# Kernel optimization log

Measured on AMD Instinct MI355X. Metric: run time of the kernel, lower is better.

Reference implementation:

```python
import jax, jax.numpy as jnp
import numpy as np

H = 16          # n_heads
MAX_REL = 512   # max_relative_positions


def setup_inputs() -> dict:
    key = jax.random.key(0)
    ks = jax.random.split(key, 8)
    B, S, D = 8, 512, 1024
    x = jax.random.normal(ks[0], (B, S, D), jnp.float32)
    rel_embeddings = jax.random.normal(ks[1], (2 * MAX_REL, D), jnp.float32) * 0.02
    Wq = jax.random.normal(ks[2], (D, D), jnp.float32) * 0.02
    Wk = jax.random.normal(ks[3], (D, D), jnp.float32) * 0.02
    Wv = jax.random.normal(ks[4], (D, D), jnp.float32) * 0.02
    bq = jnp.zeros((D,), jnp.float32)
    bk = jnp.zeros((D,), jnp.float32)
    bv = jnp.zeros((D,), jnp.float32)
    ids = jnp.arange(S)
    relative_pos = (ids[:, None] - ids[None, :]).astype(jnp.int32)  # q_id - k_id
    mask = jnp.ones((B, S), dtype=bool)
    return dict(x=x, rel_embeddings=rel_embeddings, Wq=Wq, bq=bq, Wk=Wk, bk=bk,
                Wv=Wv, bv=bv, relative_pos=relative_pos, mask=mask)


def _proj(t, W, b):
    # (..., D) -> (H, ..., W): linear + split heads + transpose_type '2013'
    y = t @ W.T + b
    y = y.reshape(*t.shape[:-1], H, y.shape[-1] // H)
    return jnp.moveaxis(y, -2, 0)


def reference(x, rel_embeddings, Wq, bq, Wk, bk, Wv, bv, relative_pos, mask):
    B, S, D = x.shape
    Wd = D // H
    span = S  # att_span = q_len
    scale = 1.0 / np.sqrt(Wd * 3.0)  # (head_size*(1+|pos_att_type|))**-0.5

    q = _proj(x, Wq, bq)  # (H,B,S,W)
    k = _proj(x, Wk, bk)
    v = _proj(x, Wv, bv)

    # relative position embeddings window [max_rel-span : max_rel+span]
    re = rel_embeddings[MAX_REL - span:MAX_REL + span]  # (2*span, D)
    pos_k = _proj(re, Wk, bk)  # (H, 2*span, W)
    pos_q = _proj(re, Wq, bq)  # (H, 2*span, W)

    # content-to-content scores
    scores = jnp.einsum('hbiw,hbjw->hbij', q, k) * scale  # (H,B,S,S)

    # c2p: query vs relative-position keys, gathered by rel index
    c2p = jnp.einsum('hbiw,hrw->hbir', q, pos_k) * scale  # (H,B,S,2*span)
    idx_c2p = jnp.clip(relative_pos + span - 1, 0, 2 * span - 1)  # (S,S)
    bias_c2p = jnp.take_along_axis(
        c2p, jnp.broadcast_to(idx_c2p[None, None], (H, B, S, S)), axis=-1)

    # p2c: key vs relative-position queries, gathered then transposed
    p2c = jnp.einsum('hbjw,hrw->hbjr', k, pos_q) * scale  # (H,B,S,2*span)
    idx_p2c = jnp.clip(-relative_pos + span - 1, 0, 2 * span - 1)
    g = jnp.take_along_axis(
        p2c, jnp.broadcast_to(idx_p2c[None, None], (H, B, S, S)), axis=-1)
    bias_p2c = jnp.swapaxes(g, -1, -2)  # (H,B,S(q),S(k))

    scores = scores + bias_c2p + bias_p2c
    scores = jnp.where(mask[None, :, None, :], scores, jnp.float32(-1e9))
    probs = jax.nn.softmax(scores, axis=-1)
    ctx = jnp.einsum('hbij,hbjw->hbiw', probs, v)  # (H,B,S,W)
    return jnp.transpose(ctx, (1, 2, 0, 3)).reshape(B, S, D)
```

## Files before the change

kernel.cpp:

```cpp
#include <hip/hip_runtime.h>


typedef __bf16 bf16_t;
typedef __bf16 bf16x8 __attribute__((ext_vector_type(8)));
typedef __bf16 bf16x4 __attribute__((ext_vector_type(4)));
typedef float  f32x4  __attribute__((ext_vector_type(4)));

#define MFMA16(a, b, c) __builtin_amdgcn_mfma_f32_16x16x32_bf16((a), (b), (c), 0, 0, 0)
#define S2SCALE 0.10411754f
#define MCONST  4.3280851f

__device__ __forceinline__ void gload_lds16(const bf16_t* g, bf16_t* lds) {
  __builtin_amdgcn_global_load_lds(
      (const __attribute__((address_space(1))) void*)g,
      (__attribute__((address_space(3))) void*)lds, 16, 0, 0);
}

__device__ __forceinline__ int kchunk(int row, int kg) {
  return row * 8 + (kg ^ (row & 7));
}

__global__ __launch_bounds__(256) void cvt_all(
    const float* __restrict__ x, const float* __restrict__ rel,
    const float* __restrict__ wq, const float* __restrict__ wk, const float* __restrict__ wv,
    bf16_t* __restrict__ out) {
  const size_t i = ((size_t)blockIdx.x * 256 + threadIdx.x) * 8;
  const float* src; size_t off;
  if (i < 4194304) { src = x; off = i; }
  else {
    size_t j = i - 4194304; int sel = (int)(j >> 20); off = j & 1048575;
    src = sel == 0 ? wq : sel == 1 ? wk : sel == 2 ? wv : rel;
  }
  float4 v0 = *reinterpret_cast<const float4*>(src + off);
  float4 v1 = *reinterpret_cast<const float4*>(src + off + 4);
  bf16x8 o;
  o[0] = (bf16_t)v0.x; o[1] = (bf16_t)v0.y; o[2] = (bf16_t)v0.z; o[3] = (bf16_t)v0.w;
  o[4] = (bf16_t)v1.x; o[5] = (bf16_t)v1.y; o[6] = (bf16_t)v1.z; o[7] = (bf16_t)v1.w;
  *reinterpret_cast<bf16x8*>(out + i) = o;
}

__device__ __forceinline__ void stage_tile(const bf16_t* base, int T, bf16_t* lds, int tid) {
#pragma unroll
  for (int i = 0; i < 2; ++i) {
    const int c = tid + i * 512;
    const int row = c >> 2, kg = (c & 3) ^ (row & 3);
    gload_lds16(base + (size_t)row * 1024 + T * 32 + kg * 8, lds + c * 8);
  }
}

#define VMW2 asm volatile("s_waitcnt vmcnt(2)" ::: "memory")
#define VMW0 asm volatile("s_waitcnt vmcnt(0)" ::: "memory")
#define NOPS ((void)0)

#define PH_BODY(AB, BB, FH, READB, STAGE_STMT, WAIT_STMT)                               \
  {                                                                                     \
    if (READB) {                                                                        \
      _Pragma("unroll") for (int n_ = 0; n_ < 4; ++n_)                                  \
        bfr[n_] = *reinterpret_cast<const bf16x8*>(                                     \
            (BB) + (((wn * 64 + n_ * 16 + li) * 4 + (gr ^ (li & 3))) * 8));             \
    }                                                                                   \
    bf16x8 af_[4];                                                                      \
    _Pragma("unroll") for (int a_ = 0; a_ < 4; ++a_)                                    \
      af_[a_] = *reinterpret_cast<const bf16x8*>(                                       \
          (AB) + (((wm * 128 + ((FH) * 4 + a_) * 16 + li) * 4 + (gr ^ (li & 3))) * 8)); \
    STAGE_STMT;                                                                         \
    __builtin_amdgcn_s_barrier();                                                       \
    asm volatile("s_waitcnt lgkmcnt(0)" ::: "memory");                                  \
    __builtin_amdgcn_sched_barrier(0);                                                  \
    __builtin_amdgcn_s_setprio(1);                                                      \
    _Pragma("unroll") for (int a_ = 0; a_ < 4; ++a_)                                    \
      _Pragma("unroll") for (int n_ = 0; n_ < 4; ++n_)                                  \
        acc[(FH) * 4 + a_][n_] = MFMA16(af_[a_], bfr[n_], acc[(FH) * 4 + a_][n_]);      \
    __builtin_amdgcn_s_setprio(0);                                                      \
    WAIT_STMT;                                                                          \
    __builtin_amdgcn_s_barrier();                                                       \
    __builtin_amdgcn_sched_barrier(0);                                                  \
  }

__global__ __launch_bounds__(512, 2) void gemm_qkv(
    const bf16_t* __restrict__ xb, const bf16_t* __restrict__ reb,
    const bf16_t* __restrict__ wqb, const bf16_t* __restrict__ wkb, const bf16_t* __restrict__ wvb,
    const float* __restrict__ bq, const float* __restrict__ bk, const float* __restrict__ bv,
    bf16_t* __restrict__ qo, bf16_t* __restrict__ ko, bf16_t* __restrict__ vo,
    bf16_t* __restrict__ pko, bf16_t* __restrict__ pqo) {
  __shared__ bf16_t Abuf[2][8192];
  __shared__ bf16_t Bbuf[2][8192];

  const int bid0 = blockIdx.x;
  const int bid = (bid0 & 7) * 28 + (bid0 >> 3);
  const int tid = threadIdx.x;
  const int wave = tid >> 6;
  const int wm = wave >> 2, wn = wave & 3;
  const int l = tid & 63, li = l & 15, gr = l >> 4;

  const bf16_t* Abase; const bf16_t* Bbase; const float* bias; float sc;
  bf16_t* Cout; int row0, col0;
  if (bid < 192) {
    const int bx = bid / 12, by = bid % 12;
    Abase = xb + (size_t)bx * 262144; row0 = bx * 256;
    const int wsel = by >> 2;
    Bbase = (wsel == 0 ? wqb : wsel == 1 ? wkb : wvb) + (size_t)(by & 3) * 262144;
    bias = wsel == 0 ? bq : wsel == 1 ? bk : bv;
    sc = wsel == 0 ? S2SCALE : 1.f;
    Cout = wsel == 0 ? qo : wsel == 1 ? ko : vo;
    col0 = (by & 3) * 256;
  } else {
    const int p = bid - 192;
    const int bx = p >> 3, by = p & 7;
    Abase = reb + (size_t)bx * 262144; row0 = bx * 256;
    const int wsel = by >> 2;
    Bbase = (wsel == 0 ? wkb : wqb) + (size_t)(by & 3) * 262144;
    bias = wsel == 0 ? bk : bq;
    sc = wsel == 0 ? 1.f : S2SCALE;
    Cout = wsel == 0 ? pko : pqo;
    col0 = (by & 3) * 256;
  }

  f32x4 acc[8][4] = {};
  bf16x8 bfr[4];

  stage_tile(Abase, 0, Abuf[0], tid);
  stage_tile(Bbase, 0, Bbuf[0], tid);
  stage_tile(Bbase, 1, Bbuf[1], tid);
  VMW2;
  __builtin_amdgcn_s_barrier();
  __builtin_amdgcn_sched_barrier(0);

  for (int t = 0; t < 15; ++t) {
    const int T0 = 2 * t;
    PH_BODY(Abuf[0], Bbuf[0], 0, true,  stage_tile(Abase, T0 + 1, Abuf[1], tid), NOPS);
    PH_BODY(Abuf[0], Bbuf[0], 1, false, stage_tile(Bbase, T0 + 2, Bbuf[0], tid), VMW2);
    PH_BODY(Abuf[1], Bbuf[1], 0, true,  stage_tile(Abase, T0 + 2, Abuf[0], tid), NOPS);
    PH_BODY(Abuf[1], Bbuf[1], 1, false, stage_tile(Bbase, T0 + 3, Bbuf[1], tid), VMW2);
  }
  PH_BODY(Abuf[0], Bbuf[0], 0, true,  stage_tile(Abase, 31, Abuf[1], tid), NOPS);
  PH_BODY(Abuf[0], Bbuf[0], 1, false, NOPS, VMW0);
  PH_BODY(Abuf[1], Bbuf[1], 0, true,  NOPS, NOPS);
  PH_BODY(Abuf[1], Bbuf[1], 1, false, NOPS, NOPS);

#pragma unroll
  for (int a = 0; a < 8; ++a)
#pragma unroll
    for (int n = 0; n < 4; ++n) {
      const int col = col0 + wn * 64 + n * 16 + li;
      const float bv_ = bias[col];
#pragma unroll
      for (int r = 0; r < 4; ++r) {
        const int row = row0 + wm * 128 + a * 16 + gr * 4 + r;
        Cout[(size_t)row * 1024 + col] = (bf16_t)((acc[a][n][r] + bv_) * sc);
      }
    }
}

__global__ __launch_bounds__(512) void attn_mega(
    const bf16_t* __restrict__ qb, const bf16_t* __restrict__ kb,
    const bf16_t* __restrict__ vb, const bf16_t* __restrict__ pkb,
    const bf16_t* __restrict__ pqb, float* __restrict__ out) {
  const int bid0 = blockIdx.x;
  const int bid = (bid0 & 7) * 64 + (bid0 >> 3);
  const int qp = bid & 3;
  const int bh = bid >> 2;
  const int h = bh & 15, b = bh >> 4;
  const int i0base = qp * 128;
  const int tid = threadIdx.x;
  const int w = tid >> 6, l = tid & 63;
  const int qh = w >> 2, wv = w & 3;
  const int li = l & 15, gr = l >> 4;
  const int i0 = i0base + qh * 64;

  __shared__ bf16_t Ks[2][4096];
  __shared__ bf16_t PKs[4][4096];
  __shared__ bf16_t PQs[4][4096];
  __shared__ bf16_t VT[4096];
  __shared__ bf16_t Pl[8][1024];
  __shared__ bf16_t DcpT[8][80][20];
  __shared__ bf16_t D2p[2][64][100];

#define STG(gsrc, lds) { int s_ = tid ^ ((tid >> 3) & 7);                              \
    gload_lds16((gsrc) + (size_t)(s_ >> 3) * 1024 + (s_ & 7) * 8, (lds) + tid * 8); }

  const bf16_t* qptr = qb + (size_t)(b * 512 + i0 + wv * 16 + li) * 1024 + h * 64 + gr * 8;
  const bf16x8 aq0 = *reinterpret_cast<const bf16x8*>(qptr);
  const bf16x8 aq1 = *reinterpret_cast<const bf16x8*>(qptr + 32);

  const bf16_t* kbase = kb + (size_t)(b * 512) * 1024 + h * 64;
  const bf16_t* vbase = vb + (size_t)(b * 512) * 1024 + h * 64;
  const bf16_t* pkw = pkb + (size_t)i0base * 1024 + h * 64;
  const bf16_t* pqw = pqb + (size_t)i0base * 1024 + h * 64;

  f32x4 acc[4] = {};
  float lsum[4] = {0.f, 0.f, 0.f, 0.f};
  bf16x8 vreg[2];

  STG(kbase, Ks[0]);
#pragma unroll
  for (int s = 7; s <= 9; ++s) {
    STG(pkw + (size_t)s * 65536, PKs[s & 3]);
    STG(pqw + (size_t)s * 65536, PQs[s & 3]);
  }
  vreg[0] = *reinterpret_cast<const bf16x8*>(vbase + (size_t)(tid >> 3) * 1024 + (tid & 7) * 8);

#pragma unroll
  for (int jt = 0; jt < 8; ++jt) {
    const int cur = jt & 1;
    const int sb = qh + 7 - jt;

    asm volatile("s_waitcnt vmcnt(0)" ::: "memory");
    __builtin_amdgcn_s_barrier();
    __builtin_amdgcn_sched_barrier(0);

    if (jt < 7) {
      STG(kbase + (size_t)(jt + 1) * 65536, Ks[cur ^ 1]);
      const int sg = 6 - jt;
      STG(pkw + (size_t)sg * 65536, PKs[sg & 3]);
      STG(pqw + (size_t)sg * 65536, PQs[sg & 3]);
      vreg[cur ^ 1] = *reinterpret_cast<const bf16x8*>(
          vbase + (size_t)((jt + 1) * 64 + (tid >> 3)) * 1024 + (tid & 7) * 8);
    }

    {
      const int j = tid >> 3, w0 = (tid & 7) * 8;
      bf16x8 vv = vreg[cur];
#pragma unroll
      for (int e = 0; e < 8; ++e) {
        int ch = (j >> 3) * 64 + w0 + e;
        ch ^= ((ch >> 3) & 7);
        VT[ch * 8 + (j & 7)] = vv[e];
      }
    }

    __builtin_amdgcn_s_setprio(1);
    f32x4 sfr[4];
#pragma unroll
    for (int n = 0; n < 4; ++n) {
      const int j_ = n * 16 + li;
      bf16x8 b0 = *reinterpret_cast<const bf16x8*>(Ks[cur] + kchunk(j_, gr) * 8);
      bf16x8 b1 = *reinterpret_cast<const bf16x8*>(Ks[cur] + kchunk(j_, 4 + gr) * 8);
      f32x4 t = {};
      t = MFMA16(aq0, b0, t);
      t = MFMA16(aq1, b1, t);
      sfr[n] = t;
    }

#pragma unroll
    for (int cg = 0; cg < 5; ++cg) {
      const int b16 = wv + cg;
      const int slot = (sb + (b16 >> 2)) & 3;
      const int r64 = (b16 & 3) * 16 + li;
      bf16x8 p0 = *reinterpret_cast<const bf16x8*>(PKs[slot] + kchunk(r64, gr) * 8);
      bf16x8 p1 = *reinterpret_cast<const bf16x8*>(PKs[slot] + kchunk(r64, 4 + gr) * 8);
      f32x4 d = {};
      d = MFMA16(aq0, p0, d);
      d = MFMA16(aq1, p1, d);
      bf16x4 dv;
#pragma unroll
      for (int r = 0; r < 4; ++r) dv[r] = (bf16_t)d[r];
      *reinterpret_cast<bf16x4*>(&DcpT[w][cg * 16 + li][gr * 4]) = dv;
    }

    const bf16x8 ak0 = *reinterpret_cast<const bf16x8*>(Ks[cur] + kchunk(wv * 16 + li, gr) * 8);
    const bf16x8 ak1 = *reinterpret_cast<const bf16x8*>(Ks[cur] + kchunk(wv * 16 + li, 4 + gr) * 8);
#pragma unroll
    for (int cg = 0; cg < 5; ++cg) {
      const int b16 = 3 - wv + cg;
      const int slot = (sb + (b16 >> 2)) & 3;
      const int r64 = (b16 & 3) * 16 + li;
      bf16x8 p0 = *reinterpret_cast<const bf16x8*>(PQs[slot] + kchunk(r64, gr) * 8);
      bf16x8 p1 = *reinterpret_cast<const bf16x8*>(PQs[slot] + kchunk(r64, 4 + gr) * 8);
      f32x4 d = {};
      d = MFMA16(ak0, p0, d);
      d = MFMA16(ak1, p1, d);
#pragma unroll
      for (int r = 0; r < 4; ++r) {
        const int jp = gr * 4 + r;
        const int c16 = cg * 16 + li + jp + 1;
        D2p[qh][wv * 16 + jp][c16] = (bf16_t)d[r];
      }
    }
    __builtin_amdgcn_s_setprio(0);

    asm volatile("s_waitcnt lgkmcnt(0)" ::: "memory");
    __builtin_amdgcn_s_barrier();
    __builtin_amdgcn_sched_barrier(0);

#pragma unroll
    for (int n = 0; n < 4; ++n) {
      const bf16x4 pvv =
          *reinterpret_cast<const bf16x4*>(&D2p[qh][n * 16 + li][wv * 16 + gr * 4 + 16]);
#pragma unroll
      for (int r = 0; r < 4; ++r) {
        const int ip = gr * 4 + r;
        const float c2 = (float)DcpT[w][ip + 63 - n * 16 - li][ip];
        const float s = sfr[n][r] + c2 + (float)pvv[r] - MCONST;
        const float pe = __builtin_amdgcn_exp2f(s);
        lsum[r] += pe;
        int ch = (n * 2 + (li >> 3)) * 16 + gr * 4 + r;
        ch ^= ((ch >> 3) & 7);
        Pl[w][ch * 8 + (li & 7)] = (bf16_t)pe;
      }
    }

    asm volatile("s_waitcnt lgkmcnt(0)" ::: "memory");
    __builtin_amdgcn_sched_barrier(0);

    __builtin_amdgcn_s_setprio(1);
#pragma unroll
    for (int ks = 0; ks < 2; ++ks) {
      int chA = (ks * 4 + gr) * 16 + li;
      chA ^= ((chA >> 3) & 7);
      bf16x8 ap = *reinterpret_cast<const bf16x8*>(Pl[w] + chA * 8);
#pragma unroll
      for (int n2 = 0; n2 < 4; ++n2) {
        int chB = (ks * 4 + gr) * 64 + n2 * 16 + li;
        chB ^= ((chB >> 3) & 7);
        bf16x8 bvf = *reinterpret_cast<const bf16x8*>(VT + chB * 8);
        acc[n2] = MFMA16(ap, bvf, acc[n2]);
      }
    }
    __builtin_amdgcn_s_setprio(0);
  }
#undef STG

#pragma unroll
  for (int mm = 1; mm < 16; mm <<= 1)
#pragma unroll
    for (int r = 0; r < 4; ++r)
      lsum[r] += __shfl_xor(lsum[r], mm, 64);
  float invl[4];
#pragma unroll
  for (int r = 0; r < 4; ++r) invl[r] = 1.0f / lsum[r];

#pragma unroll
  for (int n2 = 0; n2 < 4; ++n2)
#pragma unroll
    for (int r = 0; r < 4; ++r) {
      const int i = i0 + wv * 16 + gr * 4 + r;
      const int wcol = n2 * 16 + li;
      out[(size_t)(b * 512 + i) * 1024 + h * 64 + wcol] = acc[n2][r] * invl[r];
    }
}

extern "C" void kernel_launch(void* const* d_in, const int* in_sizes, int n_in,
                              void* d_out, int out_size, void* d_ws, size_t ws_size,
                              hipStream_t stream) {
  (void)in_sizes; (void)n_in; (void)out_size; (void)ws_size;
  const float* x   = (const float*)d_in[0];
  const float* rel = (const float*)d_in[1];
  const float* Wq  = (const float*)d_in[2];
  const float* bq  = (const float*)d_in[3];
  const float* Wk  = (const float*)d_in[4];
  const float* bk  = (const float*)d_in[5];
  const float* Wv  = (const float*)d_in[6];
  const float* bv  = (const float*)d_in[7];
  float* out = (float*)d_out;

  bf16_t* ws  = (bf16_t*)d_ws;
  bf16_t* xb  = ws;
  bf16_t* wqb = xb + 4194304;
  bf16_t* wkb = wqb + 1048576;
  bf16_t* wvb = wkb + 1048576;
  bf16_t* reb = wvb + 1048576;
  bf16_t* qbuf = reb + 1048576;
  bf16_t* kbuf = qbuf + 4194304;
  bf16_t* vbuf = kbuf + 4194304;
  bf16_t* pkb = vbuf + 4194304;
  bf16_t* pqb = pkb + 1048576;

  cvt_all<<<4096, 256, 0, stream>>>(x, rel, Wq, Wk, Wv, ws);
  gemm_qkv<<<224, 512, 0, stream>>>(xb, reb, wqb, wkb, wvb,
                                    bq, bk, bv, qbuf, kbuf, vbuf, pkb, pqb);
  attn_mega<<<512, 512, 0, stream>>>(qbuf, kbuf, vbuf, pkb, pqb, out);
}
```

Before: 108.7 us.

## Store QKV in MFMA fragment layout and read operands directly from global

The projection GEMM epilogue now writes Q, K, V and the positional projections in a pre-swizzled fragment-major layout, so each lane's MFMA operand is a contiguous 16-byte chunk. The attention kernel drops all LDS staging of K, V, PK and PQ, along with the block barriers, and loads operands straight from global/L2 into registers. Blocks shrink to 4 waves covering 64 queries, giving 1024 blocks. Each wave now computes p2c itself for all 64 keys instead of sharing it across the block. This removes LDS traffic and synchronisation but adds redundant global reads and extra p2c MFMA work, and relies on L2 to serve the repeated loads.

```diff
diff --git a/kernel.cpp b/kernel.cpp
--- a/kernel.cpp
+++ b/kernel.cpp
@@ -14,10 +14,6 @@
   __builtin_amdgcn_global_load_lds(
       (const __attribute__((address_space(1))) void*)g,
       (__attribute__((address_space(3))) void*)lds, 16, 0, 0);
-}
-
-__device__ __forceinline__ int kchunk(int row, int kg) {
-  return row * 8 + (kg ^ (row & 7));
 }
 
 __global__ __launch_bounds__(256) void cvt_all(
@@ -81,8 +77,8 @@
     const bf16_t* __restrict__ xb, const bf16_t* __restrict__ reb,
     const bf16_t* __restrict__ wqb, const bf16_t* __restrict__ wkb, const bf16_t* __restrict__ wvb,
     const float* __restrict__ bq, const float* __restrict__ bk, const float* __restrict__ bv,
-    bf16_t* __restrict__ qo, bf16_t* __restrict__ ko, bf16_t* __restrict__ vo,
-    bf16_t* __restrict__ pko, bf16_t* __restrict__ pqo) {
+    bf16_t* __restrict__ qF, bf16_t* __restrict__ kF, bf16_t* __restrict__ vF,
+    bf16_t* __restrict__ pkF, bf16_t* __restrict__ pqF) {
   __shared__ bf16_t Abuf[2][8192];
   __shared__ bf16_t Bbuf[2][8192];
 
@@ -94,7 +90,7 @@
   const int l = tid & 63, li = l & 15, gr = l >> 4;
 
   const bf16_t* Abase; const bf16_t* Bbase; const float* bias; float sc;
-  bf16_t* Cout; int row0, col0;
+  bf16_t* Cout; int row0, col0, kind;
   if (bid < 192) {
     const int bx = bid / 12, by = bid % 12;
     Abase = xb + (size_t)bx * 262144; row0 = bx * 256;
@@ -102,7 +98,8 @@
     Bbase = (wsel == 0 ? wqb : wsel == 1 ? wkb : wvb) + (size_t)(by & 3) * 262144;
     bias = wsel == 0 ? bq : wsel == 1 ? bk : bv;
     sc = wsel == 0 ? S2SCALE : 1.f;
-    Cout = wsel == 0 ? qo : wsel == 1 ? ko : vo;
+    Cout = wsel == 0 ? qF : wsel == 1 ? kF : vF;
+    kind = wsel == 2 ? 2 : 1;
     col0 = (by & 3) * 256;
   } else {
     const int p = bid - 192;
@@ -112,7 +109,8 @@
     Bbase = (wsel == 0 ? wkb : wqb) + (size_t)(by & 3) * 262144;
     bias = wsel == 0 ? bk : bq;
     sc = wsel == 0 ? 1.f : S2SCALE;
-    Cout = wsel == 0 ? pko : pqo;
+    Cout = wsel == 0 ? pkF : pqF;
+    kind = 3;
     col0 = (by & 3) * 256;
   }
 
@@ -143,112 +141,88 @@
 #pragma unroll
     for (int n = 0; n < 4; ++n) {
       const int col = col0 + wn * 64 + n * 16 + li;
+      const int h_ = col >> 6, kk = col & 63;
       const float bv_ = bias[col];
-#pragma unroll
-      for (int r = 0; r < 4; ++r) {
-        const int row = row0 + wm * 128 + a * 16 + gr * 4 + r;
-        Cout[(size_t)row * 1024 + col] = (bf16_t)((acc[a][n][r] + bv_) * sc);
+      const int rowb = row0 + wm * 128 + a * 16 + gr * 4;
+      if (kind == 2) {
+        bf16x4 ov;
+#pragma unroll
+        for (int r = 0; r < 4; ++r) ov[r] = (bf16_t)((acc[a][n][r] + bv_) * sc);
+        const int j = rowb & 511, b_ = rowb >> 9;
+        const size_t flat = ((((size_t)(b_ * 16 + h_) * 16 + (j >> 5)) * 4 + (kk >> 4)) * 512) +
+                            ((size_t)((kk & 15) | (((j >> 3) & 3) << 4))) * 8 + (j & 7);
+        *reinterpret_cast<bf16x4*>(Cout + flat) = ov;
+      } else {
+        const int ks = kk >> 5, kg3 = (kk >> 3) & 3, e = kk & 7;
+#pragma unroll
+        for (int r = 0; r < 4; ++r) {
+          const int row = rowb + r;
+          const int blk = (kind == 1) ? (((row >> 9) * 16 + h_) * 32 + ((row & 511) >> 4))
+                                      : (h_ * 64 + (row >> 4));
+          const size_t flat = ((size_t)blk * 2 + ks) * 512 + ((row & 15) | (kg3 << 4)) * 8 + e;
+          Cout[flat] = (bf16_t)((acc[a][n][r] + bv_) * sc);
+        }
       }
     }
 }
 
-__global__ __launch_bounds__(512) void attn_mega(
-    const bf16_t* __restrict__ qb, const bf16_t* __restrict__ kb,
-    const bf16_t* __restrict__ vb, const bf16_t* __restrict__ pkb,
-    const bf16_t* __restrict__ pqb, float* __restrict__ out) {
+__global__ __launch_bounds__(256, 2) void attn_v3(
+    const bf16_t* __restrict__ qF, const bf16_t* __restrict__ kF,
+    const bf16_t* __restrict__ vF, const bf16_t* __restrict__ pkF,
+    const bf16_t* __restrict__ pqF, float* __restrict__ out) {
   const int bid0 = blockIdx.x;
-  const int bid = (bid0 & 7) * 64 + (bid0 >> 3);
-  const int qp = bid & 3;
-  const int bh = bid >> 2;
-  const int h = bh & 15, b = bh >> 4;
-  const int i0base = qp * 128;
+  const int bid = (bid0 & 7) * 128 + (bid0 >> 3);
+  const int qt = bid & 7;
+  const int h = (bid >> 3) & 15;
+  const int b = bid >> 7;
+  const int i0 = qt * 64;
   const int tid = threadIdx.x;
-  const int w = tid >> 6, l = tid & 63;
-  const int qh = w >> 2, wv = w & 3;
+  const int l = tid & 63;
+  const int w = tid >> 6;
   const int li = l & 15, gr = l >> 4;
-  const int i0 = i0base + qh * 64;
-
-  __shared__ bf16_t Ks[2][4096];
-  __shared__ bf16_t PKs[4][4096];
-  __shared__ bf16_t PQs[4][4096];
-  __shared__ bf16_t VT[4096];
-  __shared__ bf16_t Pl[8][1024];
-  __shared__ bf16_t DcpT[8][80][20];
-  __shared__ bf16_t D2p[2][64][100];
-
-#define STG(gsrc, lds) { int s_ = tid ^ ((tid >> 3) & 7);                              \
-    gload_lds16((gsrc) + (size_t)(s_ >> 3) * 1024 + (s_ & 7) * 8, (lds) + tid * 8); }
-
-  const bf16_t* qptr = qb + (size_t)(b * 512 + i0 + wv * 16 + li) * 1024 + h * 64 + gr * 8;
-  const bf16x8 aq0 = *reinterpret_cast<const bf16x8*>(qptr);
-  const bf16x8 aq1 = *reinterpret_cast<const bf16x8*>(qptr + 32);
-
-  const bf16_t* kbase = kb + (size_t)(b * 512) * 1024 + h * 64;
-  const bf16_t* vbase = vb + (size_t)(b * 512) * 1024 + h * 64;
-  const bf16_t* pkw = pkb + (size_t)i0base * 1024 + h * 64;
-  const bf16_t* pqw = pqb + (size_t)i0base * 1024 + h * 64;
+
+  __shared__ bf16_t Pl[4][1024];
+  __shared__ bf16_t DcpT[4][80][20];
+  __shared__ bf16_t D2pT[4][80][68];
+
+  const bf16_t* qFb = qF + (size_t)(b * 16 + h) * 32768;
+  const bf16_t* kFb = kF + (size_t)(b * 16 + h) * 32768;
+  const bf16_t* vFb = vF + (size_t)(b * 16 + h) * 32768;
+  const bf16_t* pkFb = pkF + (size_t)h * 65536;
+  const bf16_t* pqFb = pqF + (size_t)h * 65536;
+
+  const bf16x8 aq0 = *reinterpret_cast<const bf16x8*>(qFb + ((size_t)(qt * 4 + w) * 2 + 0) * 512 + l * 8);
+  const bf16x8 aq1 = *reinterpret_cast<const bf16x8*>(qFb + ((size_t)(qt * 4 + w) * 2 + 1) * 512 + l * 8);
 
   f32x4 acc[4] = {};
   float lsum[4] = {0.f, 0.f, 0.f, 0.f};
-  bf16x8 vreg[2];
-
-  STG(kbase, Ks[0]);
-#pragma unroll
-  for (int s = 7; s <= 9; ++s) {
-    STG(pkw + (size_t)s * 65536, PKs[s & 3]);
-    STG(pqw + (size_t)s * 65536, PQs[s & 3]);
-  }
-  vreg[0] = *reinterpret_cast<const bf16x8*>(vbase + (size_t)(tid >> 3) * 1024 + (tid & 7) * 8);
-
-#pragma unroll
+
   for (int jt = 0; jt < 8; ++jt) {
-    const int cur = jt & 1;
-    const int sb = qh + 7 - jt;
-
-    asm volatile("s_waitcnt vmcnt(0)" ::: "memory");
-    __builtin_amdgcn_s_barrier();
-    __builtin_amdgcn_sched_barrier(0);
-
-    if (jt < 7) {
-      STG(kbase + (size_t)(jt + 1) * 65536, Ks[cur ^ 1]);
-      const int sg = 6 - jt;
-      STG(pkw + (size_t)sg * 65536, PKs[sg & 3]);
-      STG(pqw + (size_t)sg * 65536, PQs[sg & 3]);
-      vreg[cur ^ 1] = *reinterpret_cast<const bf16x8*>(
-          vbase + (size_t)((jt + 1) * 64 + (tid >> 3)) * 1024 + (tid & 7) * 8);
-    }
-
-    {
-      const int j = tid >> 3, w0 = (tid & 7) * 8;
-      bf16x8 vv = vreg[cur];
-#pragma unroll
-      for (int e = 0; e < 8; ++e) {
-        int ch = (j >> 3) * 64 + w0 + e;
-        ch ^= ((ch >> 3) & 7);
-        VT[ch * 8 + (j & 7)] = vv[e];
-      }
-    }
+    bf16x8 kA[4][2];
+#pragma unroll
+    for (int jb = 0; jb < 4; ++jb)
+#pragma unroll
+      for (int ks = 0; ks < 2; ++ks)
+        kA[jb][ks] = *reinterpret_cast<const bf16x8*>(
+            kFb + ((size_t)(jt * 4 + jb) * 2 + ks) * 512 + l * 8);
+
+    const int db0 = 4 * qt - 4 * jt + 28 + w;
 
     __builtin_amdgcn_s_setprio(1);
     f32x4 sfr[4];
 #pragma unroll
     for (int n = 0; n < 4; ++n) {
-      const int j_ = n * 16 + li;
-      bf16x8 b0 = *reinterpret_cast<const bf16x8*>(Ks[cur] + kchunk(j_, gr) * 8);
-      bf16x8 b1 = *reinterpret_cast<const bf16x8*>(Ks[cur] + kchunk(j_, 4 + gr) * 8);
       f32x4 t = {};
-      t = MFMA16(aq0, b0, t);
-      t = MFMA16(aq1, b1, t);
+      t = MFMA16(aq0, kA[n][0], t);
+      t = MFMA16(aq1, kA[n][1], t);
       sfr[n] = t;
     }
 
 #pragma unroll
     for (int cg = 0; cg < 5; ++cg) {
-      const int b16 = wv + cg;
-      const int slot = (sb + (b16 >> 2)) & 3;
-      const int r64 = (b16 & 3) * 16 + li;
-      bf16x8 p0 = *reinterpret_cast<const bf16x8*>(PKs[slot] + kchunk(r64, gr) * 8);
-      bf16x8 p1 = *reinterpret_cast<const bf16x8*>(PKs[slot] + kchunk(r64, 4 + gr) * 8);
+      const bf16_t* pp = pkFb + ((size_t)(db0 + cg) * 2) * 512 + l * 8;
+      bf16x8 p0 = *reinterpret_cast<const bf16x8*>(pp);
+      bf16x8 p1 = *reinterpret_cast<const bf16x8*>(pp + 512);
       f32x4 d = {};
       d = MFMA16(aq0, p0, d);
       d = MFMA16(aq1, p1, d);
@@ -258,40 +232,33 @@
       *reinterpret_cast<bf16x4*>(&DcpT[w][cg * 16 + li][gr * 4]) = dv;
     }
 
-    const bf16x8 ak0 = *reinterpret_cast<const bf16x8*>(Ks[cur] + kchunk(wv * 16 + li, gr) * 8);
-    const bf16x8 ak1 = *reinterpret_cast<const bf16x8*>(Ks[cur] + kchunk(wv * 16 + li, 4 + gr) * 8);
 #pragma unroll
     for (int cg = 0; cg < 5; ++cg) {
-      const int b16 = 3 - wv + cg;
-      const int slot = (sb + (b16 >> 2)) & 3;
-      const int r64 = (b16 & 3) * 16 + li;
-      bf16x8 p0 = *reinterpret_cast<const bf16x8*>(PQs[slot] + kchunk(r64, gr) * 8);
-      bf16x8 p1 = *reinterpret_cast<const bf16x8*>(PQs[slot] + kchunk(r64, 4 + gr) * 8);
-      f32x4 d = {};
-      d = MFMA16(ak0, p0, d);
-      d = MFMA16(ak1, p1, d);
-#pragma unroll
-      for (int r = 0; r < 4; ++r) {
-        const int jp = gr * 4 + r;
-        const int c16 = cg * 16 + li + jp + 1;
-        D2p[qh][wv * 16 + jp][c16] = (bf16_t)d[r];
+      const bf16_t* qq = pqFb + ((size_t)(db0 + cg) * 2) * 512 + l * 8;
+      bf16x8 q0 = *reinterpret_cast<const bf16x8*>(qq);
+      bf16x8 q1 = *reinterpret_cast<const bf16x8*>(qq + 512);
+#pragma unroll
+      for (int jb = 0; jb < 4; ++jb) {
+        f32x4 d = {};
+        d = MFMA16(kA[jb][0], q0, d);
+        d = MFMA16(kA[jb][1], q1, d);
+        bf16x4 dv;
+#pragma unroll
+        for (int r = 0; r < 4; ++r) dv[r] = (bf16_t)d[r];
+        *reinterpret_cast<bf16x4*>(&D2pT[w][cg * 16 + li][jb * 16 + gr * 4]) = dv;
       }
     }
     __builtin_amdgcn_s_setprio(0);
 
-    asm volatile("s_waitcnt lgkmcnt(0)" ::: "memory");
-    __builtin_amdgcn_s_barrier();
-    __builtin_amdgcn_sched_barrier(0);
-
 #pragma unroll
     for (int n = 0; n < 4; ++n) {
-      const bf16x4 pvv =
-          *reinterpret_cast<const bf16x4*>(&D2p[qh][n * 16 + li][wv * 16 + gr * 4 + 16]);
 #pragma unroll
       for (int r = 0; r < 4; ++r) {
         const int ip = gr * 4 + r;
-        const float c2 = (float)DcpT[w][ip + 63 - n * 16 - li][ip];
-        const float s = sfr[n][r] + c2 + (float)pvv[r] - MCONST;
+        const int u = ip + 63 - n * 16 - li;
+        const float c2 = (float)DcpT[w][u][ip];
+        const float p2 = (float)D2pT[w][u][n * 16 + li];
+        const float s = sfr[n][r] + c2 + p2 - MCONST;
         const float pe = __builtin_amdgcn_exp2f(s);
         lsum[r] += pe;
         int ch = (n * 2 + (li >> 3)) * 16 + gr * 4 + r;
@@ -300,9 +267,6 @@
       }
     }
 
-    asm volatile("s_waitcnt lgkmcnt(0)" ::: "memory");
-    __builtin_amdgcn_sched_barrier(0);
-
     __builtin_amdgcn_s_setprio(1);
 #pragma unroll
     for (int ks = 0; ks < 2; ++ks) {
@@ -311,15 +275,13 @@
       bf16x8 ap = *reinterpret_cast<const bf16x8*>(Pl[w] + chA * 8);
 #pragma unroll
       for (int n2 = 0; n2 < 4; ++n2) {
-        int chB = (ks * 4 + gr) * 64 + n2 * 16 + li;
-        chB ^= ((chB >> 3) & 7);
-        bf16x8 bvf = *reinterpret_cast<const bf16x8*>(VT + chB * 8);
+        bf16x8 bvf = *reinterpret_cast<const bf16x8*>(
+            vFb + (((size_t)(jt * 2 + ks) * 4 + n2) * 512) + l * 8);
         acc[n2] = MFMA16(ap, bvf, acc[n2]);
       }
     }
     __builtin_amdgcn_s_setprio(0);
   }
-#undef STG
 
 #pragma unroll
   for (int mm = 1; mm < 16; mm <<= 1)
@@ -334,7 +296,7 @@
   for (int n2 = 0; n2 < 4; ++n2)
 #pragma unroll
     for (int r = 0; r < 4; ++r) {
-      const int i = i0 + wv * 16 + gr * 4 + r;
+      const int i = i0 + w * 16 + gr * 4 + r;
       const int wcol = n2 * 16 + li;
       out[(size_t)(b * 512 + i) * 1024 + h * 64 + wcol] = acc[n2][r] * invl[r];
     }
@@ -360,14 +322,14 @@
   bf16_t* wkb = wqb + 1048576;
   bf16_t* wvb = wkb + 1048576;
   bf16_t* reb = wvb + 1048576;
-  bf16_t* qbuf = reb + 1048576;
-  bf16_t* kbuf = qbuf + 4194304;
-  bf16_t* vbuf = kbuf + 4194304;
-  bf16_t* pkb = vbuf + 4194304;
-  bf16_t* pqb = pkb + 1048576;
+  bf16_t* qFb = reb + 1048576;
+  bf16_t* kFb = qFb + 4194304;
+  bf16_t* vFb = kFb + 4194304;
+  bf16_t* pkFb = vFb + 4194304;
+  bf16_t* pqFb = pkFb + 1048576;
 
   cvt_all<<<4096, 256, 0, stream>>>(x, rel, Wq, Wk, Wv, ws);
   gemm_qkv<<<224, 512, 0, stream>>>(xb, reb, wqb, wkb, wvb,
-                                    bq, bk, bv, qbuf, kbuf, vbuf, pkb, pqb);
-  attn_mega<<<512, 512, 0, stream>>>(qbuf, kbuf, vbuf, pkb, pqb, out);
-}
+                                    bq, bk, bv, qFb, kFb, vFb, pkFb, pqFb);
+  attn_v3<<<1024, 256, 0, stream>>>(qFb, kFb, vFb, pkFb, pqFb, out);
+}
```

Result: slower. 116.4 us (+7.1%).
